# Kernel optimization log

Measured on AMD Instinct MI355X. Metric: run time of the kernel, lower is better.

## Reference

```python
import jax, jax.numpy as jnp
import numpy as np

N_NODES = 100000
N_EDGES = 1600000
D = 128


def _deg_inv_sqrt(idx, num_nodes):
    deg = jax.ops.segment_sum(jnp.ones_like(idx, dtype=jnp.float32), idx, num_segments=num_nodes)
    deg = jnp.clip(deg, 1.0, None)  # DGL clamps degree to min 1
    return deg ** -0.5


def graph_conv(x, W, b, src, dst, out_norm, in_norm, relu):
    # norm='both': scale by src out-degree^{-1/2}, transform, aggregate, scale by dst in-degree^{-1/2}
    h = x * out_norm[:, None]
    h = h @ W                               # [N, d_out]
    m = jax.ops.segment_sum(h[src], dst, num_segments=x.shape[0])  # sparse A^T h
    m = m * in_norm[:, None] + b
    return jax.nn.relu(m) if relu else m


def setup_inputs() -> dict:
    key = jax.random.key(0)
    ks = jax.random.split(key, 8)
    s = 1.0 / np.sqrt(D)
    return {
        "node_feats": jax.random.normal(ks[0], (N_NODES, D), dtype=jnp.float32),
        "src": jax.random.randint(ks[1], (N_EDGES,), 0, N_NODES, dtype=jnp.int32),
        "dst": jax.random.randint(ks[2], (N_EDGES,), 0, N_NODES, dtype=jnp.int32),
        "W1": jax.random.normal(ks[3], (D, D), dtype=jnp.float32) * s,
        "b1": jnp.zeros((D,), jnp.float32),
        "W2": jax.random.normal(ks[4], (D, D), dtype=jnp.float32) * s,
        "b2": jnp.zeros((D,), jnp.float32),
        "res_W": jax.random.normal(ks[5], (D, D), dtype=jnp.float32) * s,
        "mlp_W": jax.random.normal(ks[6], (D, 2), dtype=jnp.float32) * s,
        "mlp_b": jnp.zeros((2,), jnp.float32),
    }


def reference(node_feats, src, dst, W1, b1, W2, b2, res_W, mlp_W, mlp_b):
    out_norm = _deg_inv_sqrt(src, node_feats.shape[0])  # out-degree of source nodes
    in_norm = _deg_inv_sqrt(dst, node_feats.shape[0])   # in-degree of dest nodes
    h = graph_conv(node_feats, W1, b1, src, dst, out_norm, in_norm, relu=True)
    # dropout p=0.0 -> identity
    h = graph_conv(h, W2, b2, src, dst, out_norm, in_norm, relu=False)
    # residual (res_fc is Linear without bias)
    h = h + node_feats @ res_W
    # final MLP head -> logits [N, 2]
    return h @ mlp_W + mlp_b
```

## Files before the change

### kernel.cpp

```cpp
#include <hip/hip_runtime.h>
#include <stdint.h>

__device__ __forceinline__ float bflo(unsigned int u) {
    union { unsigned int u; float f; } c; c.u = u << 16; return c.f;
}
__device__ __forceinline__ unsigned int f2bf(float f) {
    union { float f; unsigned int u; } c; c.f = f;
    unsigned int u = c.u;
    u += 0x7fffu + ((u >> 16) & 1u);
    return u >> 16;
}
__device__ __forceinline__ unsigned int packbf(float a, float b) {
    return f2bf(a) | (f2bf(b) << 16);
}

typedef __attribute__((ext_vector_type(8))) short s8v;
typedef __attribute__((ext_vector_type(4))) float f4v;
typedef __attribute__((ext_vector_type(2))) float f2v;

__device__ __forceinline__ f4v mfma16(s8v a, s8v b, f4v c) {
    return __builtin_amdgcn_mfma_f32_16x16x32_bf16(a, b, c, 0, 0, 0);
}

__device__ __forceinline__ unsigned char f2fp8(float v) {
    return (unsigned char)(__builtin_amdgcn_cvt_pk_fp8_f32(v, v, 0, false) & 0xff);
}

#define RANGE_BITS 15
#define RANGE (1 << RANGE_BITS)
#define NR 4
#define NSLICE 64

__global__ __launch_bounds__(256) void k_prep_w(const float* __restrict__ W1,
                                                unsigned short* __restrict__ Wt) {
    const float* W = W1;
    unsigned short* T = Wt;
    const int wv = threadIdx.x >> 6, l = threadIdx.x & 63;
    const int kb = blockIdx.y * 32 + wv * 8;
#pragma unroll
    for (int half = 0; half < 2; ++half) {
        const int n = l + half * 64;
        unsigned short tmp[8];
#pragma unroll
        for (int j = 0; j < 8; ++j) tmp[j] = (unsigned short)f2bf(W[(size_t)(kb + j) * 128 + n]);
#pragma unroll
        for (int j = 0; j < 8; j += 2)
            *(unsigned int*)&T[(size_t)n * 128 + kb + j] =
                (unsigned int)tmp[j] | ((unsigned int)tmp[j + 1] << 16);
    }
}

__global__ __launch_bounds__(128) void k_prep_g(const float* __restrict__ Wr,
                                                const float* __restrict__ W2,
                                                const float* __restrict__ mlpW,
                                                float* __restrict__ G) {
    const float* W = blockIdx.x ? W2 : Wr;
    float* o = G + blockIdx.x * 256;
    const int k = threadIdx.x;
    float g0 = 0.f, g1 = 0.f;
    for (int j = 0; j < 128; ++j) {
        const float w = W[k * 128 + j];
        g0 = fmaf(w, mlpW[j * 2 + 0], g0);
        g1 = fmaf(w, mlpW[j * 2 + 1], g1);
    }
    o[k * 2 + 0] = g0;
    o[k * 2 + 1] = g1;
}

__global__ __launch_bounds__(64) void k_prep_k(const float* __restrict__ b2,
                                               const float* __restrict__ mlpW,
                                               const float* __restrict__ mlpB,
                                               float* __restrict__ K) {
    const int l = threadIdx.x;
    float p0 = b2[l] * mlpW[l * 2 + 0] + b2[l + 64] * mlpW[(l + 64) * 2 + 0];
    float p1 = b2[l] * mlpW[l * 2 + 1] + b2[l + 64] * mlpW[(l + 64) * 2 + 1];
#pragma unroll
    for (int off = 32; off > 0; off >>= 1) {
        p0 += __shfl_xor(p0, off);
        p1 += __shfl_xor(p1, off);
    }
    if (l == 0) { K[0] = p0 + mlpB[0]; K[1] = p1 + mlpB[1]; }
}

__global__ __launch_bounds__(256) void k_hist_lds(const int* __restrict__ src,
                                                  const int* __restrict__ dst,
                                                  unsigned int* __restrict__ partialS,
                                                  unsigned int* __restrict__ partialD,
                                                  int E, int EPS) {
    __shared__ unsigned int cnt[RANGE / 2];
    const int r = blockIdx.x & (NR - 1);
    const int s = blockIdx.x >> 2;
    const int a = blockIdx.y;
    const int* __restrict__ arr = a ? dst : src;
    unsigned int* part = (a ? partialD : partialS)
                         + ((size_t)r * NSLICE + s) * (RANGE / 2);
    for (int i = threadIdx.x; i < RANGE / 2; i += 256) cnt[i] = 0;
    __syncthreads();
    const int e0 = s * EPS;
    const int e1 = min(E, e0 + EPS);
    int e = e0 + threadIdx.x * 4;
    for (; e + 3 < e1; e += 1024) {
        const int4 v = *(const int4*)&arr[e];
        if ((v.x >> RANGE_BITS) == r) { int l = v.x & (RANGE - 1); atomicAdd(&cnt[l >> 1], 1u << ((l & 1) << 4)); }
        if ((v.y >> RANGE_BITS) == r) { int l = v.y & (RANGE - 1); atomicAdd(&cnt[l >> 1], 1u << ((l & 1) << 4)); }
        if ((v.z >> RANGE_BITS) == r) { int l = v.z & (RANGE - 1); atomicAdd(&cnt[l >> 1], 1u << ((l & 1) << 4)); }
        if ((v.w >> RANGE_BITS) == r) { int l = v.w & (RANGE - 1); atomicAdd(&cnt[l >> 1], 1u << ((l & 1) << 4)); }
    }
    for (; e < e1; ++e) {
        const int idx = arr[e];
        if ((idx >> RANGE_BITS) == r) { int l = idx & (RANGE - 1); atomicAdd(&cnt[l >> 1], 1u << ((l & 1) << 4)); }
    }
    __syncthreads();
    for (int i = threadIdx.x; i < RANGE / 2; i += 256) part[i] = cnt[i];
}

__global__ __launch_bounds__(256) void k_deg_reduce(unsigned int* __restrict__ pS,
                                                    unsigned int* __restrict__ pD,
                                                    float* __restrict__ out_norm,
                                                    float* __restrict__ in_norm,
                                                    int* __restrict__ in_deg, int N) {
    const int a = blockIdx.y;
    const int t = blockIdx.x * 256 + threadIdx.x;
    const int r = t >> (RANGE_BITS - 1);
    const int w = t & ((RANGE / 2) - 1);
    unsigned int* base = (a ? pD : pS) + (size_t)r * NSLICE * (RANGE / 2) + w;
    unsigned int lo = 0, hi = 0;
    if (a) {
        for (int s = 0; s < NSLICE; ++s) {
            const unsigned int v = base[(size_t)s * (RANGE / 2)];
            base[(size_t)s * (RANGE / 2)] = lo | (hi << 16);
            lo += v & 0xffffu; hi += v >> 16;
        }
    } else {
        for (int s = 0; s < NSLICE; ++s) {
            const unsigned int v = base[(size_t)s * (RANGE / 2)];
            lo += v & 0xffffu; hi += v >> 16;
        }
    }
    const int n0 = r * RANGE + 2 * w, n1 = n0 + 1;
    if (a) {
        if (n0 < N) { in_deg[n0] = (int)lo; in_norm[n0] = rsqrtf(fmaxf((float)lo, 1.f)); }
        if (n1 < N) { in_deg[n1] = (int)hi; in_norm[n1] = rsqrtf(fmaxf((float)hi, 1.f)); }
    } else {
        if (n0 < N) out_norm[n0] = rsqrtf(fmaxf((float)lo, 1.f));
        if (n1 < N) out_norm[n1] = rsqrtf(fmaxf((float)hi, 1.f));
    }
}

__global__ __launch_bounds__(1024) void k_scan_block(const int* __restrict__ in,
                                                     int* __restrict__ row_ptr,
                                                     int* __restrict__ partials, int n) {
    __shared__ int sh[1024];
    int i = blockIdx.x * 1024 + threadIdx.x;
    int v = (i < n) ? in[i] : 0;
    sh[threadIdx.x] = v;
    __syncthreads();
    for (int off = 1; off < 1024; off <<= 1) {
        int t = (threadIdx.x >= off) ? sh[threadIdx.x - off] : 0;
        __syncthreads();
        sh[threadIdx.x] += t;
        __syncthreads();
    }
    if (i < n) row_ptr[i + 1] = sh[threadIdx.x];
    if (threadIdx.x == 1023) partials[blockIdx.x] = sh[1023];
}

__global__ __launch_bounds__(1024) void k_scan_partials(int* __restrict__ partials, int nb) {
    __shared__ int sh[1024];
    int v = (threadIdx.x < nb) ? partials[threadIdx.x] : 0;
    sh[threadIdx.x] = v;
    __syncthreads();
    for (int off = 1; off < 1024; off <<= 1) {
        int t = (threadIdx.x >= off) ? sh[threadIdx.x - off] : 0;
        __syncthreads();
        sh[threadIdx.x] += t;
        __syncthreads();
    }
    if (threadIdx.x < nb) partials[threadIdx.x] = sh[threadIdx.x] - v;
}

__global__ void k_scan_finalize(int* __restrict__ row_ptr, const int* __restrict__ partials,
                                int n) {
    int i = blockIdx.x * blockDim.x + threadIdx.x;
    if (i < n) {
        row_ptr[i + 1] += partials[i >> 10];
        if (i == 0) row_ptr[0] = 0;
    }
}

__global__ __launch_bounds__(256) void k_scatter_lds(const int* __restrict__ src,
                                                     const int* __restrict__ dst,
                                                     const unsigned int* __restrict__ pD,
                                                     const int* __restrict__ row_ptr,
                                                     int* __restrict__ ssrc, int E, int EPS) {
    __shared__ unsigned int cur[RANGE / 2];
    const int r = blockIdx.x & (NR - 1);
    const int s = blockIdx.x >> 2;
    const unsigned int* pre = pD + ((size_t)r * NSLICE + s) * (RANGE / 2);
    for (int i = threadIdx.x; i < RANGE / 2; i += 256) cur[i] = pre[i];
    __syncthreads();
    const int e0 = s * EPS;
    const int e1 = min(E, e0 + EPS);
    int e = e0 + threadIdx.x * 4;
    for (; e + 3 < e1; e += 1024) {
        const int4 v = *(const int4*)&dst[e];
#pragma unroll
        for (int j = 0; j < 4; ++j) {
            const int d = (&v.x)[j];
            if ((d >> RANGE_BITS) == r) {
                const int local = d & (RANGE - 1);
                const int sh = (local & 1) << 4;
                const unsigned int old = atomicAdd(&cur[local >> 1], 1u << sh);
                const unsigned int off = (old >> sh) & 0xffffu;
                ssrc[row_ptr[d] + (int)off] = src[e + j];
            }
        }
    }
    for (; e < e1; ++e) {
        const int d = dst[e];
        if ((d >> RANGE_BITS) == r) {
            const int local = d & (RANGE - 1);
            const int sh = (local & 1) << 4;
            const unsigned int old = atomicAdd(&cur[local >> 1], 1u << sh);
            const unsigned int off = (old >> sh) & 0xffffu;
            ssrc[row_ptr[d] + (int)off] = src[e];
        }
    }
}

__global__ __launch_bounds__(256) void k_gemm1(const float* __restrict__ X,
                                               const unsigned short* __restrict__ Wt0,
                                               const float* __restrict__ scale,
                                               const float* __restrict__ G,
                                               unsigned char* __restrict__ out_table,
                                               float2* __restrict__ outv,
                                               int N) {
    __shared__ unsigned short Ws[128 * 128];
    __shared__ float2 gr[128];
    const int tid = threadIdx.x;
    for (int i = tid; i < 2048; i += 256) {
        const int n = i >> 4, b = i & 15;
        const uint4 v = *(const uint4*)&Wt0[(size_t)n * 128 + b * 8];
        *(uint4*)&Ws[n * 128 + ((b ^ (n & 15)) << 3)] = v;
    }
    if (tid < 128) gr[tid] = ((const float2*)G)[tid];
    __syncthreads();

    const int lane = tid & 63;
    const int wave = tid >> 6;
    const int quad = lane >> 4;
    const int l16 = lane & 15;
    const int r_base = blockIdx.x * 64 + wave * 16;
    const int ra = min(r_base + l16, N - 1);

    f4v acc[8];
#pragma unroll
    for (int nn = 0; nn < 8; ++nn) acc[nn] = (f4v)0.f;
    float p0 = 0.f, p1 = 0.f;

    const float* xp = X + (size_t)ra * 128 + quad * 8;

#pragma unroll
    for (int kt = 0; kt < 4; ++kt) {
        const float4 lo = *(const float4*)(xp + kt * 32);
        const float4 hi = *(const float4*)(xp + kt * 32 + 4);
        {
            const int kb = kt * 32 + quad * 8;
            const float xv[8] = {lo.x, lo.y, lo.z, lo.w, hi.x, hi.y, hi.z, hi.w};
#pragma unroll
            for (int j = 0; j < 8; ++j) {
                const float2 g = gr[kb + j];
                p0 = fmaf(xv[j], g.x, p0);
                p1 = fmaf(xv[j], g.y, p1);
            }
        }
        s8v af;
        af[0] = (short)f2bf(lo.x); af[1] = (short)f2bf(lo.y);
        af[2] = (short)f2bf(lo.z); af[3] = (short)f2bf(lo.w);
        af[4] = (short)f2bf(hi.x); af[5] = (short)f2bf(hi.y);
        af[6] = (short)f2bf(hi.z); af[7] = (short)f2bf(hi.w);
#pragma unroll
        for (int nn = 0; nn < 8; ++nn) {
            const int bofs = (nn * 16 + l16) * 128 + (((kt * 4 + quad) ^ l16) << 3);
            const s8v bf = *(const s8v*)&Ws[bofs];
            acc[nn] = mfma16(af, bf, acc[nn]);
        }
    }

    p0 += __shfl_xor(p0, 16); p0 += __shfl_xor(p0, 32);
    p1 += __shfl_xor(p1, 16); p1 += __shfl_xor(p1, 32);
    if (quad == 0 && r_base + l16 < N) outv[r_base + l16] = make_float2(p0, p1);

    const int rc = r_base + quad * 4;
    float sc[4];
#pragma unroll
    for (int g = 0; g < 4; ++g) sc[g] = scale[min(rc + g, N - 1)];
#pragma unroll
    for (int nn = 0; nn < 8; ++nn) {
        const int col = nn * 16 + l16;
#pragma unroll
        for (int g = 0; g < 4; ++g) {
            const int r = rc + g;
            if (r < N) out_table[(size_t)r * 128 + col] = f2fp8(acc[nn][g] * sc[g]);
        }
    }
}

__global__ __launch_bounds__(256) void k_spmm1(const unsigned char* __restrict__ T,
                                               const int* __restrict__ row_ptr,
                                               const int* __restrict__ ssrc,
                                               const float* __restrict__ in_norm,
                                               const float* __restrict__ bias,
                                               unsigned short* __restrict__ Hout, int N) {
    const int lane = threadIdx.x & 63;
    const int grp = lane >> 4;
    const int gl  = lane & 15;
    const int d = blockIdx.x * 4 + (threadIdx.x >> 6);
    if (d >= N) return;

    const int start = row_ptr[d], end = row_ptr[d + 1];
    float acc[8];
#pragma unroll
    for (int j = 0; j < 8; ++j) acc[j] = 0.f;

    for (int base = start; base < end; base += 64) {
        const int cnt = min(64, end - base);
        const int sl = (lane < cnt) ? ssrc[base + lane] : 0;
        for (int i = 0; i < cnt; i += 16) {
            int   ss[4];
            float mm[4];
            uint2 ww[4];
#pragma unroll
            for (int u = 0; u < 4; ++u) {
                const int e = i + 4 * u + grp;
                ss[u] = __shfl(sl, min(e, cnt - 1));
                mm[u] = (e < cnt) ? 1.f : 0.f;
            }
#pragma unroll
            for (int u = 0; u < 4; ++u)
                ww[u] = *(const uint2*)&T[(size_t)ss[u] * 128 + gl * 8];
#pragma unroll
            for (int u = 0; u < 4; ++u) {
                const f2v a0 = __builtin_amdgcn_cvt_pk_f32_fp8(ww[u].x, false);
                const f2v a1 = __builtin_amdgcn_cvt_pk_f32_fp8(ww[u].x, true);
                const f2v a2 = __builtin_amdgcn_cvt_pk_f32_fp8(ww[u].y, false);
                const f2v a3 = __builtin_amdgcn_cvt_pk_f32_fp8(ww[u].y, true);
                const float m = mm[u];
                acc[0] = fmaf(m, a0[0], acc[0]); acc[1] = fmaf(m, a0[1], acc[1]);
                acc[2] = fmaf(m, a1[0], acc[2]); acc[3] = fmaf(m, a1[1], acc[3]);
                acc[4] = fmaf(m, a2[0], acc[4]); acc[5] = fmaf(m, a2[1], acc[5]);
                acc[6] = fmaf(m, a3[0], acc[6]); acc[7] = fmaf(m, a3[1], acc[7]);
            }
        }
    }

#pragma unroll
    for (int j = 0; j < 8; ++j) {
        acc[j] += __shfl_xor(acc[j], 16);
        acc[j] += __shfl_xor(acc[j], 32);
    }

    const float inr = in_norm[d];
    const float4 bb0 = *(const float4*)&bias[gl * 8];
    const float4 bb1 = *(const float4*)&bias[gl * 8 + 4];
    float v[8];
    v[0] = fmaxf(acc[0] * inr + bb0.x, 0.f); v[1] = fmaxf(acc[1] * inr + bb0.y, 0.f);
    v[2] = fmaxf(acc[2] * inr + bb0.z, 0.f); v[3] = fmaxf(acc[3] * inr + bb0.w, 0.f);
    v[4] = fmaxf(acc[4] * inr + bb1.x, 0.f); v[5] = fmaxf(acc[5] * inr + bb1.y, 0.f);
    v[6] = fmaxf(acc[6] * inr + bb1.z, 0.f); v[7] = fmaxf(acc[7] * inr + bb1.w, 0.f);

    if (grp == 0) {
        uint4 o;
        o.x = packbf(v[0], v[1]); o.y = packbf(v[2], v[3]);
        o.z = packbf(v[4], v[5]); o.w = packbf(v[6], v[7]);
        *(uint4*)&Hout[(size_t)d * 128 + gl * 8] = o;
    }
}

__global__ __launch_bounds__(256) void k_gemv2(const unsigned short* __restrict__ B,
                                               const float* __restrict__ onorm,
                                               const float* __restrict__ G,
                                               float2* __restrict__ u2, int N) {
    const int tid = threadIdx.x;
    const int lane = tid & 63;
    const int gl = lane & 15;
    const int rg = lane >> 4;
    const int row = blockIdx.x * 16 + (tid >> 6) * 4 + rg;
    const float2* G2 = (const float2*)(G + 256);
    float p0 = 0.f, p1 = 0.f;
    if (row < N) {
        const s8v bv = *(const s8v*)&B[(size_t)row * 128 + gl * 8];
#pragma unroll
        for (int j = 0; j < 8; ++j) {
            const float xv = bflo((unsigned int)(unsigned short)bv[j]);
            const float2 g = G2[gl * 8 + j];
            p0 = fmaf(xv, g.x, p0);
            p1 = fmaf(xv, g.y, p1);
        }
    }
#pragma unroll
    for (int off = 1; off < 16; off <<= 1) {
        p0 += __shfl_xor(p0, off);
        p1 += __shfl_xor(p1, off);
    }
    if (gl == 0 && row < N) {
        const float s = onorm[row];
        u2[row] = make_float2(p0 * s, p1 * s);
    }
}

__global__ __launch_bounds__(256) void k_final(const float2* __restrict__ u,
                                               const int* __restrict__ row_ptr,
                                               const int* __restrict__ ssrc,
                                               const float* __restrict__ in_norm,
                                               const float2* __restrict__ v,
                                               const float* __restrict__ K,
                                               float2* __restrict__ out, int N) {
    const int d = blockIdx.x * 256 + threadIdx.x;
    if (d >= N) return;
    const int start = row_ptr[d], end = row_ptr[d + 1];
    float sx = 0.f, sy = 0.f;
    int i = start;
    for (; i + 4 <= end; i += 4) {
        const int s0 = ssrc[i], s1 = ssrc[i + 1], s2 = ssrc[i + 2], s3 = ssrc[i + 3];
        const float2 u0 = u[s0], u1 = u[s1], u2 = u[s2], u3 = u[s3];
        sx += (u0.x + u1.x) + (u2.x + u3.x);
        sy += (u0.y + u1.y) + (u2.y + u3.y);
    }
    for (; i < end; ++i) {
        const float2 uu = u[ssrc[i]];
        sx += uu.x; sy += uu.y;
    }
    const float inr = in_norm[d];
    const float2 vv = v[d];
    out[d] = make_float2(sx * inr + vv.x + K[0], sy * inr + vv.y + K[1]);
}

extern "C" void kernel_launch(void* const* d_in, const int* in_sizes, int n_in,
                              void* d_out, int out_size, void* d_ws, size_t ws_size,
                              hipStream_t stream) {
    const float* x     = (const float*)d_in[0];
    const int*   src   = (const int*)d_in[1];
    const int*   dst   = (const int*)d_in[2];
    const float* W1    = (const float*)d_in[3];
    const float* b1    = (const float*)d_in[4];
    const float* W2    = (const float*)d_in[5];
    const float* b2    = (const float*)d_in[6];
    const float* res_W = (const float*)d_in[7];
    const float* mlp_W = (const float*)d_in[8];
    const float* mlp_b = (const float*)d_in[9];
    float* out = (float*)d_out;

    const int N = in_sizes[0] / 128;
    const int E = in_sizes[1];
    const int EPS = (E + NSLICE - 1) / NSLICE;

    char* p = (char*)d_ws;
    unsigned char*  A = (unsigned char*)p;   p += (size_t)N * 128;
    unsigned short* B = (unsigned short*)p;  p += (size_t)N * 128 * 2;
    unsigned short* Wt = (unsigned short*)p; p += (size_t)3 * 16384 * 2;
    float* out_norm = (float*)p;             p += (size_t)N * 4;
    float* in_norm  = (float*)p;             p += (size_t)N * 4;
    int* in_deg     = (int*)p;               p += (size_t)N * 4;
    int* row_ptr    = (int*)p;               p += (size_t)(N + 1) * 4;
    int* scanpart   = (int*)p;               p += (size_t)1024 * 4;
    float* Kc       = (float*)p;             p += (size_t)16;
    float2* v2      = (float2*)p;            p += (size_t)N * 8;
    float2* u2      = (float2*)p;            p += (size_t)N * 8;
    int* ssrc       = (int*)p;               p += (size_t)E * 4;
    unsigned int* partialS = (unsigned int*)A;
    unsigned int* partialD = (unsigned int*)((char*)B + (size_t)4 * 1024 * 1024);
    float* G = (float*)(scanpart + 512);

    const int gN = (N + 255) / 256;
    const int nb = (N + 1023) / 1024;
    const int gGemm = (N + 63) / 64;
    const int gSpmm = (N + 3) / 4;
    const int gGemv = (N + 15) / 16;

    k_prep_w<<<dim3(1, 4), 256, 0, stream>>>(W1, Wt);
    k_prep_g<<<2, 128, 0, stream>>>(res_W, W2, mlp_W, G);
    k_prep_k<<<1, 64, 0, stream>>>(b2, mlp_W, mlp_b, Kc);

    k_hist_lds<<<dim3(NR * NSLICE, 2), 256, 0, stream>>>(src, dst, partialS, partialD, E, EPS);
    k_deg_reduce<<<dim3(NR * (RANGE / 2) / 256, 2), 256, 0, stream>>>(partialS, partialD,
                                                                      out_norm, in_norm, in_deg, N);

    k_scan_block<<<nb, 1024, 0, stream>>>(in_deg, row_ptr, scanpart, N);
    k_scan_partials<<<1, 1024, 0, stream>>>(scanpart, nb);
    k_scan_finalize<<<gN, 256, 0, stream>>>(row_ptr, scanpart, N);
    k_scatter_lds<<<NR * NSLICE, 256, 0, stream>>>(src, dst, partialD, row_ptr, ssrc, E, EPS);

    k_gemm1<<<gGemm, 256, 0, stream>>>(x, Wt, out_norm, G, A, v2, N);

    k_spmm1<<<gSpmm, 256, 0, stream>>>(A, row_ptr, ssrc, in_norm, b1, B, N);

    k_gemv2<<<gGemv, 256, 0, stream>>>(B, out_norm, G, u2, N);

    k_final<<<gN, 256, 0, stream>>>(u2, row_ptr, ssrc, in_norm, v2, Kc, (float2*)out, N);

    (void)n_in; (void)out_size; (void)ws_size;
}
```

Baseline: 265.9 us.

## Fuse second-layer GEMV into SpMM epilogue and simplify edge gather loop

The SpMM kernel now directly computes the projection of its ReLU output onto the precomputed 2-column matrix and writes the scaled float2 result, removing the separate GEMV kernel and the bf16 hidden-feature buffer round trip. The gather loop is rewritten to have each lane group read source indices directly with stride 4, two edges per iteration, instead of batching indices via shuffles and masked FMAs. This saves a large intermediate write/read and one launch, at the cost of more scattered index loads per lane.

```diff
diff --git a/kernel.cpp b/kernel.cpp
--- a/kernel.cpp
+++ b/kernel.cpp
@@ -9,9 +9,6 @@
     unsigned int u = c.u;
     u += 0x7fffu + ((u >> 16) & 1u);
     return u >> 16;
-}
-__device__ __forceinline__ unsigned int packbf(float a, float b) {
-    return f2bf(a) | (f2bf(b) << 16);
 }
 
 typedef __attribute__((ext_vector_type(8))) short s8v;
@@ -310,8 +307,10 @@
                                                const int* __restrict__ row_ptr,
                                                const int* __restrict__ ssrc,
                                                const float* __restrict__ in_norm,
+                                               const float* __restrict__ onorm,
                                                const float* __restrict__ bias,
-                                               unsigned short* __restrict__ Hout, int N) {
+                                               const float* __restrict__ G,
+                                               float2* __restrict__ u2, int N) {
     const int lane = threadIdx.x & 63;
     const int grp = lane >> 4;
     const int gl  = lane & 15;
@@ -323,35 +322,38 @@
 #pragma unroll
     for (int j = 0; j < 8; ++j) acc[j] = 0.f;
 
-    for (int base = start; base < end; base += 64) {
-        const int cnt = min(64, end - base);
-        const int sl = (lane < cnt) ? ssrc[base + lane] : 0;
-        for (int i = 0; i < cnt; i += 16) {
-            int   ss[4];
-            float mm[4];
-            uint2 ww[4];
-#pragma unroll
-            for (int u = 0; u < 4; ++u) {
-                const int e = i + 4 * u + grp;
-                ss[u] = __shfl(sl, min(e, cnt - 1));
-                mm[u] = (e < cnt) ? 1.f : 0.f;
-            }
-#pragma unroll
-            for (int u = 0; u < 4; ++u)
-                ww[u] = *(const uint2*)&T[(size_t)ss[u] * 128 + gl * 8];
-#pragma unroll
-            for (int u = 0; u < 4; ++u) {
-                const f2v a0 = __builtin_amdgcn_cvt_pk_f32_fp8(ww[u].x, false);
-                const f2v a1 = __builtin_amdgcn_cvt_pk_f32_fp8(ww[u].x, true);
-                const f2v a2 = __builtin_amdgcn_cvt_pk_f32_fp8(ww[u].y, false);
-                const f2v a3 = __builtin_amdgcn_cvt_pk_f32_fp8(ww[u].y, true);
-                const float m = mm[u];
-                acc[0] = fmaf(m, a0[0], acc[0]); acc[1] = fmaf(m, a0[1], acc[1]);
-                acc[2] = fmaf(m, a1[0], acc[2]); acc[3] = fmaf(m, a1[1], acc[3]);
-                acc[4] = fmaf(m, a2[0], acc[4]); acc[5] = fmaf(m, a2[1], acc[5]);
-                acc[6] = fmaf(m, a3[0], acc[6]); acc[7] = fmaf(m, a3[1], acc[7]);
-            }
-        }
+    int e = start + grp;
+    for (; e + 4 < end; e += 8) {
+        const int s0 = ssrc[e];
+        const int s1 = ssrc[e + 4];
+        const uint2 w0 = *(const uint2*)&T[(size_t)(unsigned)s0 * 128 + gl * 8];
+        const uint2 w1 = *(const uint2*)&T[(size_t)(unsigned)s1 * 128 + gl * 8];
+        {
+            const f2v a0 = __builtin_amdgcn_cvt_pk_f32_fp8(w0.x, false);
+            const f2v a1 = __builtin_amdgcn_cvt_pk_f32_fp8(w0.x, true);
+            const f2v a2 = __builtin_amdgcn_cvt_pk_f32_fp8(w0.y, false);
+            const f2v a3 = __builtin_amdgcn_cvt_pk_f32_fp8(w0.y, true);
+            acc[0] += a0[0]; acc[1] += a0[1]; acc[2] += a1[0]; acc[3] += a1[1];
+            acc[4] += a2[0]; acc[5] += a2[1]; acc[6] += a3[0]; acc[7] += a3[1];
+        }
+        {
+            const f2v a0 = __builtin_amdgcn_cvt_pk_f32_fp8(w1.x, false);
+            const f2v a1 = __builtin_amdgcn_cvt_pk_f32_fp8(w1.x, true);
+            const f2v a2 = __builtin_amdgcn_cvt_pk_f32_fp8(w1.y, false);
+            const f2v a3 = __builtin_amdgcn_cvt_pk_f32_fp8(w1.y, true);
+            acc[0] += a0[0]; acc[1] += a0[1]; acc[2] += a1[0]; acc[3] += a1[1];
+            acc[4] += a2[0]; acc[5] += a2[1]; acc[6] += a3[0]; acc[7] += a3[1];
+        }
+    }
+    if (e < end) {
+        const int s0 = ssrc[e];
+        const uint2 w0 = *(const uint2*)&T[(size_t)(unsigned)s0 * 128 + gl * 8];
+        const f2v a0 = __builtin_amdgcn_cvt_pk_f32_fp8(w0.x, false);
+        const f2v a1 = __builtin_amdgcn_cvt_pk_f32_fp8(w0.x, true);
+        const f2v a2 = __builtin_amdgcn_cvt_pk_f32_fp8(w0.y, false);
+        const f2v a3 = __builtin_amdgcn_cvt_pk_f32_fp8(w0.y, true);
+        acc[0] += a0[0]; acc[1] += a0[1]; acc[2] += a1[0]; acc[3] += a1[1];
+        acc[4] += a2[0]; acc[5] += a2[1]; acc[6] += a3[0]; acc[7] += a3[1];
     }
 
 #pragma unroll
@@ -369,43 +371,22 @@
     v[4] = fmaxf(acc[4] * inr + bb1.x, 0.f); v[5] = fmaxf(acc[5] * inr + bb1.y, 0.f);
     v[6] = fmaxf(acc[6] * inr + bb1.z, 0.f); v[7] = fmaxf(acc[7] * inr + bb1.w, 0.f);
 
-    if (grp == 0) {
-        uint4 o;
-        o.x = packbf(v[0], v[1]); o.y = packbf(v[2], v[3]);
-        o.z = packbf(v[4], v[5]); o.w = packbf(v[6], v[7]);
-        *(uint4*)&Hout[(size_t)d * 128 + gl * 8] = o;
-    }
-}
-
-__global__ __launch_bounds__(256) void k_gemv2(const unsigned short* __restrict__ B,
-                                               const float* __restrict__ onorm,
-                                               const float* __restrict__ G,
-                                               float2* __restrict__ u2, int N) {
-    const int tid = threadIdx.x;
-    const int lane = tid & 63;
-    const int gl = lane & 15;
-    const int rg = lane >> 4;
-    const int row = blockIdx.x * 16 + (tid >> 6) * 4 + rg;
     const float2* G2 = (const float2*)(G + 256);
     float p0 = 0.f, p1 = 0.f;
-    if (row < N) {
-        const s8v bv = *(const s8v*)&B[(size_t)row * 128 + gl * 8];
-#pragma unroll
-        for (int j = 0; j < 8; ++j) {
-            const float xv = bflo((unsigned int)(unsigned short)bv[j]);
-            const float2 g = G2[gl * 8 + j];
-            p0 = fmaf(xv, g.x, p0);
-            p1 = fmaf(xv, g.y, p1);
-        }
+#pragma unroll
+    for (int j = 0; j < 8; ++j) {
+        const float2 g = G2[gl * 8 + j];
+        p0 = fmaf(v[j], g.x, p0);
+        p1 = fmaf(v[j], g.y, p1);
     }
 #pragma unroll
     for (int off = 1; off < 16; off <<= 1) {
         p0 += __shfl_xor(p0, off);
         p1 += __shfl_xor(p1, off);
     }
-    if (gl == 0 && row < N) {
-        const float s = onorm[row];
-        u2[row] = make_float2(p0 * s, p1 * s);
+    if (lane == 0) {
+        const float s = onorm[d];
+        u2[d] = make_float2(p0 * s, p1 * s);
     }
 }
 
@@ -476,7 +457,6 @@
     const int nb = (N + 1023) / 1024;
     const int gGemm = (N + 63) / 64;
     const int gSpmm = (N + 3) / 4;
-    const int gGemv = (N + 15) / 16;
 
     k_prep_w<<<dim3(1, 4), 256, 0, stream>>>(W1, Wt);
     k_prep_g<<<2, 128, 0, stream>>>(res_W, W2, mlp_W, G);
@@ -493,9 +473,7 @@
 
     k_gemm1<<<gGemm, 256, 0, stream>>>(x, Wt, out_norm, G, A, v2, N);
 
-    k_spmm1<<<gSpmm, 256, 0, stream>>>(A, row_ptr, ssrc, in_norm, b1, B, N);
-
-    k_gemv2<<<gGemv, 256, 0, stream>>>(B, out_norm, G, u2, N);
+    k_spmm1<<<gSpmm, 256, 0, stream>>>(A, row_ptr, ssrc, in_norm, out_norm, b1, G, u2, N);
 
     k_final<<<gN, 256, 0, stream>>>(u2, row_ptr, ssrc, in_norm, v2, Kc, (float2*)out, N);
 
```

After: 275.3 us. 3.5% more time.
